# Kernel optimization log

Measured on AMD Instinct MI355X. Metric: run time of the kernel, lower is better.

The kernel has to match this reference:

```python
import jax, jax.numpy as jnp
import numpy as np

NUM_HEADS = 16
ROPE_THETA = 10000.0


def _rope_angles(seq_len, head_dim, dtype):
    # lucidrains rotary_embedding_torch: freqs = theta^(-2i/d) for i in 0..d/2,
    # angles = pos * freq, then each angle repeated twice along last dim (interleaved pairs).
    inv_freq = 1.0 / (ROPE_THETA ** (jnp.arange(0, head_dim, 2, dtype=jnp.float32) / head_dim))
    angles = jnp.arange(seq_len, dtype=jnp.float32)[:, None] * inv_freq  # [N, D/2]
    return jnp.repeat(angles, 2, axis=-1).astype(dtype)  # [N, D]


def _rotate_half(t):
    # interleaved pairs: (x0, x1) -> (-x1, x0)
    t1 = t[..., ::2]
    t2 = t[..., 1::2]
    return jnp.stack([-t2, t1], axis=-1).reshape(t.shape)


def _apply_rope(t, cos, sin):
    # t: [B, H, N, D]; cos/sin: [N, D]
    return t * cos + _rotate_half(t) * sin


def setup_inputs() -> dict:
    key = jax.random.key(0)
    ks = jax.random.split(key, 5)
    B, N, C = 4, 1024, 1024
    return {
        "x": jax.random.normal(ks[0], (B, N, C), dtype=jnp.float32),
        "w_qkv": jax.random.normal(ks[1], (C, 3 * C), dtype=jnp.float32) * (C ** -0.5),
        "b_qkv": jax.random.normal(ks[2], (3 * C,), dtype=jnp.float32) * 0.02,
        "w_proj": jax.random.normal(ks[3], (C, C), dtype=jnp.float32) * (C ** -0.5),
        "b_proj": jax.random.normal(ks[4], (C,), dtype=jnp.float32) * 0.02,
    }


def reference(x, w_qkv, b_qkv, w_proj, b_proj):
    B, N, C = x.shape
    H = NUM_HEADS
    D = C // H

    qkv = x @ w_qkv + b_qkv  # [B, N, 3C]
    qkv = qkv.reshape(B, N, 3, H, D).transpose(2, 0, 3, 1, 4)  # [3, B, H, N, D]
    q, k, v = qkv[0], qkv[1], qkv[2]

    ang = _rope_angles(N, D, x.dtype)
    cos, sin = jnp.cos(ang), jnp.sin(ang)
    q = _apply_rope(q, cos, sin)
    k = _apply_rope(k, cos, sin)

    scale = D ** -0.5  # SDPA default scale
    scores = jnp.einsum("bhqd,bhkd->bhqk", q, k) * scale
    attn = jax.nn.softmax(scores, axis=-1)
    out = jnp.einsum("bhqk,bhkd->bhqd", attn, v)  # [B, H, N, D]

    out = out.transpose(0, 2, 1, 3).reshape(B, N, C)
    return out @ w_proj + b_proj
```

## Files before the change

### kernel.cpp

```cpp
#include <hip/hip_runtime.h>
#include <math.h>

#define BB 4
#define NN 1024
#define CC 1024
#define HH 16
#define DD 64
#define N3 3072

typedef __attribute__((ext_vector_type(8))) short bf16x8;
typedef __attribute__((ext_vector_type(8))) _Float16 f16x8;
typedef __attribute__((ext_vector_type(4))) _Float16 f16x4;
typedef __attribute__((ext_vector_type(4))) float f32x4;
typedef __attribute__((ext_vector_type(4))) unsigned int u32x4;
typedef __attribute__((ext_vector_type(2))) unsigned int u32x2;

struct ushort4_t { unsigned short x, y, z, w; };

static __device__ __forceinline__ unsigned short f2b(float f) {
    union { float f; unsigned int u; } v; v.f = f;
    unsigned int r = (v.u + 0x7fffu + ((v.u >> 16) & 1u)) >> 16;
    return (unsigned short)r;
}

static __device__ __forceinline__ void ldg_lds16(const void* g, void* l) {
    __builtin_amdgcn_global_load_lds(
        (const __attribute__((address_space(1))) unsigned int*)g,
        (__attribute__((address_space(3))) unsigned int*)l, 16, 0, 0);
}

static __device__ __forceinline__ void barx()  { asm volatile("s_barrier" ::: "memory"); }
static __device__ __forceinline__ void wlg0()  { asm volatile("s_waitcnt lgkmcnt(0)" ::: "memory");
                                                 __builtin_amdgcn_sched_barrier(0); }
static __device__ __forceinline__ void wvm8()  { asm volatile("s_waitcnt vmcnt(8)" ::: "memory"); }
static __device__ __forceinline__ void wvm4()  { asm volatile("s_waitcnt vmcnt(4)" ::: "memory"); }
static __device__ __forceinline__ void wvm0()  { asm volatile("s_waitcnt vmcnt(0)" ::: "memory"); }
static __device__ __forceinline__ void wnone() {}

__global__ __launch_bounds__(256) void prep(const float* __restrict__ x,
                                            const float* __restrict__ wq,
                                            const float* __restrict__ wp,
                                            _Float16* __restrict__ Xh,
                                            _Float16* __restrict__ Wqt,
                                            _Float16* __restrict__ Wpt,
                                            float* __restrict__ ct,
                                            float* __restrict__ st) {
    __shared__ __align__(16) _Float16 T[64][72];
    const int blk = blockIdx.x;
    const int t = threadIdx.x;
    if (blk < 4096) {
        int tid = blk * 256 + t;
        float4 v = ((const float4*)x)[tid];
        f16x4 o = {(_Float16)v.x, (_Float16)v.y, (_Float16)v.z, (_Float16)v.w};
        ((f16x4*)Xh)[tid] = o;
    } else if (blk < 5120) {
        const float* src; _Float16* dst; int ns, k0, n0;
        if (blk < 4864) {
            int idx = blk - 4096;
            k0 = (idx & 15) * 64; n0 = (idx >> 4) * 64;
            src = wq; dst = Wqt; ns = N3;
        } else {
            int idx = blk - 4864;
            k0 = (idx & 15) * 64; n0 = (idx >> 4) * 64;
            src = wp; dst = Wpt; ns = 1024;
        }
        {
            const int r  = t >> 2;
            const int cf = (t & 3) * 16;
            const float* sp = src + (size_t)(k0 + r) * ns + n0 + cf;
            float4 v0 = *(const float4*)(sp);
            float4 v1 = *(const float4*)(sp + 4);
            float4 v2 = *(const float4*)(sp + 8);
            float4 v3 = *(const float4*)(sp + 12);
            f16x8 a, b;
            a[0]=(_Float16)v0.x; a[1]=(_Float16)v0.y; a[2]=(_Float16)v0.z; a[3]=(_Float16)v0.w;
            a[4]=(_Float16)v1.x; a[5]=(_Float16)v1.y; a[6]=(_Float16)v1.z; a[7]=(_Float16)v1.w;
            b[0]=(_Float16)v2.x; b[1]=(_Float16)v2.y; b[2]=(_Float16)v2.z; b[3]=(_Float16)v2.w;
            b[4]=(_Float16)v3.x; b[5]=(_Float16)v3.y; b[6]=(_Float16)v3.z; b[7]=(_Float16)v3.w;
            *(f16x8*)&T[r][cf]     = a;
            *(f16x8*)&T[r][cf + 8] = b;
        }
        __syncthreads();
        {
            const int n  = t >> 2;
            const int kc = t & 3;
            f16x8 o0, o1;
            #pragma unroll
            for (int kk = 0; kk < 8; kk++) o0[kk] = T[kc * 16 + kk][n];
            #pragma unroll
            for (int kk = 0; kk < 8; kk++) o1[kk] = T[kc * 16 + 8 + kk][n];
            _Float16* dp = dst + (size_t)(n0 + n) * 1024 + k0 + kc * 16;
            *(f16x8*)dp       = o0;
            *(f16x8*)(dp + 8) = o1;
        }
    } else {
        int tid = (blk - 5120) * 256 + t;
        int n = tid >> 5, i = tid & 31;
        double ang = (double)n * exp2(-(double)i * (13.287712379549449 / 32.0));
        ct[tid] = (float)cos(ang);
        st[tid] = (float)sin(ang);
    }
}

__global__ __launch_bounds__(512, 2) void qkv_mfma(const _Float16* __restrict__ Ah,
                                                   const _Float16* __restrict__ Bt,
                                                   const float* __restrict__ bias,
                                                   const float* __restrict__ cost,
                                                   const float* __restrict__ sint,
                                                   unsigned short* __restrict__ Q,
                                                   unsigned short* __restrict__ K,
                                                   unsigned short* __restrict__ Vtg) {
    __shared__ __align__(16) _Float16 LA[4][128 * 64];
    __shared__ __align__(16) _Float16 LB[4][128 * 64];

    const int t    = threadIdx.x;
    const int lane = t & 63;
    const int w    = t >> 6;
    const int ln   = lane & 15, qd = lane >> 4;
    const int n0   = blockIdx.x * 256;
    const int m0   = blockIdx.y * 256;
    const int wm   = (w >> 2) * 128;
    const int wn   = (w & 3) * 64;

    const int L0 = t >> 3, hc0 = (t & 7) ^ (L0 & 7);
    const int row0 = 2 * L0 + (hc0 >> 2), co0 = (hc0 & 3) * 16;
    const int pp = 512 + t;
    const int L1 = pp >> 3, hc1 = (pp & 7) ^ (L1 & 7);
    const int row1 = 2 * L1 + (hc1 >> 2), co1 = (hc1 & 3) * 16;

    const char* gA = (const char*)Ah;
    const char* gB = (const char*)Bt;
    const size_t aof0 = (size_t)(m0 + row0) * 2048 + co0;
    const size_t aof1 = (size_t)(m0 + row1) * 2048 + co1;
    const size_t bof0 = (size_t)(n0 + row0) * 2048 + co0;
    const size_t bof1 = (size_t)(n0 + row1) * 2048 + co1;
    const int ld0 = (w * 64) * 8;
    const int ld1 = (512 + w * 64) * 8;

#define STAGE_A(kk, SLOT) { ldg_lds16(gA + aof0 + (size_t)(kk) * 64, &LA[SLOT][ld0]); \
                            ldg_lds16(gA + aof1 + (size_t)(kk) * 64, &LA[SLOT][ld1]); }
#define STAGE_B(kk, SLOT) { ldg_lds16(gB + bof0 + (size_t)(kk) * 64, &LB[SLOT][ld0]); \
                            ldg_lds16(gB + bof1 + (size_t)(kk) * 64, &LB[SLOT][ld1]); }

    STAGE_A(0, 0); STAGE_B(0, 0);
    STAGE_A(1, 1); STAGE_B(1, 1);
    STAGE_A(2, 2); STAGE_B(2, 2);
    wvm8();
    barx();

    f32x4 acc[8][4];
    #pragma unroll
    for (int i = 0; i < 8; i++)
        #pragma unroll
        for (int j = 0; j < 4; j++) acc[i][j] = (f32x4){0.f, 0.f, 0.f, 0.f};

    auto frag = [&](const _Float16* Lb, int r, int c) -> f16x8 {
        int idx = ((r >> 1) << 6) + ((((((r & 1) << 2) | c)) ^ ((r >> 1) & 7)) << 3);
        return *(const f16x8*)&Lb[idx];
    };

#define QK_TILE(kk, SLOT, STG, WAITFN) {                                            \
    const _Float16* Ab = LA[SLOT];                                                  \
    const _Float16* Bb = LB[SLOT];                                                  \
    f16x8 af[4], bf[4];                                                             \
    _Pragma("unroll") for (int i = 0; i < 4; i++) af[i] = frag(Ab, wm + i * 16 + ln, qd); \
    _Pragma("unroll") for (int j = 0; j < 4; j++) bf[j] = frag(Bb, wn + j * 16 + ln, qd); \
    if (STG) STAGE_A((kk) + 3, ((kk) + 3) & 3);                                     \
    barx(); wlg0();                                                                 \
    __builtin_amdgcn_s_setprio(1);                                                  \
    _Pragma("unroll") for (int i = 0; i < 4; i++)                                   \
        _Pragma("unroll") for (int j = 0; j < 4; j++)                               \
            acc[i][j] = __builtin_amdgcn_mfma_f32_16x16x32_f16(af[i], bf[j], acc[i][j], 0, 0, 0); \
    __builtin_amdgcn_s_setprio(0);                                                  \
    barx();                                                                         \
    _Pragma("unroll") for (int i = 0; i < 4; i++) af[i] = frag(Ab, wm + 64 + i * 16 + ln, qd); \
    if (STG) STAGE_B((kk) + 3, ((kk) + 3) & 3);                                     \
    WAITFN();                                                                       \
    barx(); wlg0();                                                                 \
    __builtin_amdgcn_s_setprio(1);                                                  \
    _Pragma("unroll") for (int i = 0; i < 4; i++)                                   \
        _Pragma("unroll") for (int j = 0; j < 4; j++)                               \
            acc[4 + i][j] = __builtin_amdgcn_mfma_f32_16x16x32_f16(af[i], bf[j], acc[4 + i][j], 0, 0, 0); \
    __builtin_amdgcn_s_setprio(0);                                                  \
    barx();                                                                         \
}

    for (int k = 0; k < 28; k += 4) {
        QK_TILE(k + 0, 0, 1, wvm8);
        QK_TILE(k + 1, 1, 1, wvm8);
        QK_TILE(k + 2, 2, 1, wvm8);
        QK_TILE(k + 3, 3, 1, wvm8);
    }
    QK_TILE(28, 0, 1, wvm8);
    QK_TILE(29, 1, 0, wvm4);
    QK_TILE(30, 2, 0, wvm0);
    QK_TILE(31, 3, 0, wnone);

#undef QK_TILE
#undef STAGE_A
#undef STAGE_B

    float* LW = (float*)(&LA[0][0]) + w * (16 * 68);
    const int s = (n0 + wn) >> 10;
    const int h = ((n0 + wn) >> 6) & 15;
    const int erow = lane >> 2;
    const int ec0  = (lane & 3) * 16;

    if (s < 2) {
        unsigned short* dst = (s == 0) ? Q : K;
        const float sc0 = (s == 0) ? 0.125f : 1.0f;
        f32x4 bb0 = *(const f32x4*)&bias[n0 + wn + ec0 + 0];
        f32x4 bb1 = *(const f32x4*)&bias[n0 + wn + ec0 + 4];
        f32x4 bb2 = *(const f32x4*)&bias[n0 + wn + ec0 + 8];
        f32x4 bb3 = *(const f32x4*)&bias[n0 + wn + ec0 + 12];
        #pragma unroll
        for (int i = 0; i < 8; i++) {
            #pragma unroll
            for (int j = 0; j < 4; j++)
                #pragma unroll
                for (int reg = 0; reg < 4; reg++)
                    LW[(qd * 4 + reg) * 68 + j * 16 + ln] = acc[i][j][reg];
            wlg0();
            f32x4 v0 = *(const f32x4*)&LW[erow * 68 + ec0 + 0];
            f32x4 v1 = *(const f32x4*)&LW[erow * 68 + ec0 + 4];
            f32x4 v2 = *(const f32x4*)&LW[erow * 68 + ec0 + 8];
            f32x4 v3 = *(const f32x4*)&LW[erow * 68 + ec0 + 12];
            wlg0();
            int row = m0 + wm + i * 16 + erow;
            int b = row >> 10, n = row & 1023;
            f32x4 cs0 = *(const f32x4*)&cost[n * 32 + (ec0 >> 1)];
            f32x4 cs1 = *(const f32x4*)&cost[n * 32 + (ec0 >> 1) + 4];
            f32x4 sn0 = *(const f32x4*)&sint[n * 32 + (ec0 >> 1)];
            f32x4 sn1 = *(const f32x4*)&sint[n * 32 + (ec0 >> 1) + 4];
            cs0 *= sc0; cs1 *= sc0; sn0 *= sc0; sn1 *= sc0;
            v0 += bb0; v1 += bb1; v2 += bb2; v3 += bb3;
            unsigned int pk0, pk1, pk2, pk3, pk4, pk5, pk6, pk7;
#define RP(PK, ve, vo, cs, sn) { float oe = (ve) * (cs) - (vo) * (sn);              \
                                 float oo = (vo) * (cs) + (ve) * (sn);              \
            asm("v_cvt_pk_bf16_f32 %0, %1, %2" : "=v"(PK) : "v"(oe), "v"(oo)); }
            RP(pk0, v0[0], v0[1], cs0[0], sn0[0]);
            RP(pk1, v0[2], v0[3], cs0[1], sn0[1]);
            RP(pk2, v1[0], v1[1], cs0[2], sn0[2]);
            RP(pk3, v1[2], v1[3], cs0[3], sn0[3]);
            RP(pk4, v2[0], v2[1], cs1[0], sn1[0]);
            RP(pk5, v2[2], v2[3], cs1[1], sn1[1]);
            RP(pk6, v3[0], v3[1], cs1[2], sn1[2]);
            RP(pk7, v3[2], v3[3], cs1[3], sn1[3]);
#undef RP
            unsigned short* op = dst + (((size_t)(b * HH + h)) * NN + n) * DD + ec0;
            u32x4 o0; o0[0] = pk0; o0[1] = pk1; o0[2] = pk2; o0[3] = pk3;
            u32x4 o1; o1[0] = pk4; o1[1] = pk5; o1[2] = pk6; o1[3] = pk7;
            *(u32x4*)op = o0;
            *(u32x4*)(op + 8) = o1;
        }
    } else {
        const float bb = bias[n0 + wn + lane];
        #pragma unroll
        for (int i = 0; i < 8; i++) {
            #pragma unroll
            for (int j = 0; j < 4; j++)
                #pragma unroll
                for (int reg = 0; reg < 4; reg++)
                    LW[(qd * 4 + reg) * 68 + j * 16 + ln] = acc[i][j][reg];
            wlg0();
            float e0  = LW[ 0 * 68 + lane] + bb, e1  = LW[ 1 * 68 + lane] + bb;
            float e2  = LW[ 2 * 68 + lane] + bb, e3  = LW[ 3 * 68 + lane] + bb;
            float e4  = LW[ 4 * 68 + lane] + bb, e5  = LW[ 5 * 68 + lane] + bb;
            float e6  = LW[ 6 * 68 + lane] + bb, e7  = LW[ 7 * 68 + lane] + bb;
            float e8  = LW[ 8 * 68 + lane] + bb, e9  = LW[ 9 * 68 + lane] + bb;
            float e10 = LW[10 * 68 + lane] + bb, e11 = LW[11 * 68 + lane] + bb;
            float e12 = LW[12 * 68 + lane] + bb, e13 = LW[13 * 68 + lane] + bb;
            float e14 = LW[14 * 68 + lane] + bb, e15 = LW[15 * 68 + lane] + bb;
            wlg0();
            unsigned int pk0, pk1, pk2, pk3, pk4, pk5, pk6, pk7;
#define CV(PK, a, b_) asm("v_cvt_pk_bf16_f32 %0, %1, %2" : "=v"(PK) : "v"(a), "v"(b_))
            CV(pk0, e0,  e1);  CV(pk1, e2,  e3);
            CV(pk2, e4,  e5);  CV(pk3, e6,  e7);
            CV(pk4, e8,  e9);  CV(pk5, e10, e11);
            CV(pk6, e12, e13); CV(pk7, e14, e15);
#undef CV
            int row0v = m0 + wm + i * 16;
            int b = row0v >> 10, nn = row0v & 1023;
            unsigned short* vp = Vtg + ((size_t)(b * HH + h) * DD + lane) * NN + nn;
            u32x4 o0; o0[0] = pk0; o0[1] = pk1; o0[2] = pk2; o0[3] = pk3;
            u32x4 o1; o1[0] = pk4; o1[1] = pk5; o1[2] = pk6; o1[3] = pk7;
            *(u32x4*)vp = o0;
            *(u32x4*)(vp + 8) = o1;
        }
    }
}

static __device__ __forceinline__ void gemm_body_pipe_n64(const char* gA, const char* gB,
                                                          int m0, int n0,
                                                          _Float16* As0, _Float16* As1,
                                                          _Float16* Bs0, _Float16* Bs1,
                                                          int tid, int ln, int qd,
                                                          int wm, int wn, f32x4 acc[4][2]) {
    const int lrow   = tid >> 3;
    const int lchunk = tid & 7;
    const int swz    = (lchunk ^ (lrow & 7)) * 8;

    u32x4 pa[4], pb[2];

    #pragma unroll
    for (int c = 0; c < 4; c++)
        pa[c] = *(const u32x4*)(gA + (size_t)(m0 + c * 32 + lrow) * 2048 + lchunk * 16);
    #pragma unroll
    for (int c = 0; c < 2; c++)
        pb[c] = *(const u32x4*)(gB + (size_t)(n0 + c * 32 + lrow) * 2048 + lchunk * 16);
    #pragma unroll
    for (int c = 0; c < 4; c++)
        *(u32x4*)&As0[(c * 32 + lrow) * 64 + swz] = pa[c];
    #pragma unroll
    for (int c = 0; c < 2; c++)
        *(u32x4*)&Bs0[(c * 32 + lrow) * 64 + swz] = pb[c];
    #pragma unroll
    for (int c = 0; c < 4; c++)
        pa[c] = *(const u32x4*)(gA + (size_t)(m0 + c * 32 + lrow) * 2048 + 128 + lchunk * 16);
    #pragma unroll
    for (int c = 0; c < 2; c++)
        pb[c] = *(const u32x4*)(gB + (size_t)(n0 + c * 32 + lrow) * 2048 + 128 + lchunk * 16);
    __syncthreads();

    #pragma unroll
    for (int t = 0; t < 16; t++) {
        const _Float16* Ac = (t & 1) ? As1 : As0;
        const _Float16* Bc = (t & 1) ? Bs1 : Bs0;

        #pragma unroll
        for (int kc = 0; kc < 2; kc++) {
            f16x8 af[4], bf[2];
            #pragma unroll
            for (int i = 0; i < 4; i++)
                af[i] = *(const f16x8*)&Ac[(wm + i * 16 + ln) * 64 +
                                           (((kc * 4 + qd) ^ (ln & 7)) * 8)];
            #pragma unroll
            for (int j = 0; j < 2; j++)
                bf[j] = *(const f16x8*)&Bc[(wn + j * 16 + ln) * 64 +
                                           (((kc * 4 + qd) ^ (ln & 7)) * 8)];
            #pragma unroll
            for (int i = 0; i < 4; i++)
                #pragma unroll
                for (int j = 0; j < 2; j++)
                    acc[i][j] = __builtin_amdgcn_mfma_f32_16x16x32_f16(af[i], bf[j],
                                                                       acc[i][j], 0, 0, 0);
        }

        if (t < 15) {
            _Float16* An = (t & 1) ? As0 : As1;
            _Float16* Bn = (t & 1) ? Bs0 : Bs1;
            #pragma unroll
            for (int c = 0; c < 4; c++)
                *(u32x4*)&An[(c * 32 + lrow) * 64 + swz] = pa[c];
            #pragma unroll
            for (int c = 0; c < 2; c++)
                *(u32x4*)&Bn[(c * 32 + lrow) * 64 + swz] = pb[c];
            if (t < 14) {
                size_t ko = (size_t)(t + 2) * 128;
                #pragma unroll
                for (int c = 0; c < 4; c++)
                    pa[c] = *(const u32x4*)(gA + (size_t)(m0 + c * 32 + lrow) * 2048 + ko + lchunk * 16);
                #pragma unroll
                for (int c = 0; c < 2; c++)
                    pb[c] = *(const u32x4*)(gB + (size_t)(n0 + c * 32 + lrow) * 2048 + ko + lchunk * 16);
            }
        }
        __syncthreads();
    }
}

__global__ __launch_bounds__(256, 2) void attn_flash(const unsigned short* __restrict__ Qb,
                                                     const unsigned short* __restrict__ Kb,
                                                     const unsigned short* __restrict__ Vtg,
                                                     _Float16* __restrict__ AO) {
    __shared__ __align__(16) unsigned short Ps[4][32 * 64];

    const int t    = threadIdx.x;
    const int lane = t & 63;
    const int w    = t >> 6;
    const int ln   = lane & 15;
    const int qd   = lane >> 4;

    const int lin  = blockIdx.x;
    const int slot = lin >> 3;
    const int hb   = (lin & 7) + 8 * (slot & 7);
    const int bq   = slot >> 3;
    const int h    = hb & 15;
    const int b    = hb >> 4;

    const size_t base = (size_t)(b * HH + h) * NN * DD;
    const char* Kc = (const char*)(Kb + base);
    const char* Vc = (const char*)(Vtg + base);

    bf16x8 qf[2][2];
    #pragma unroll
    for (int g = 0; g < 2; g++) {
        const unsigned short* qp = Qb + base +
            (size_t)(bq * 128 + w * 32 + g * 16 + ln) * DD + qd * 8;
        qf[g][0] = *(const bf16x8*)qp;
        qf[g][1] = *(const bf16x8*)(qp + 32);
    }

    f32x4 o[2][5];
    #pragma unroll
    for (int g = 0; g < 2; g++)
        #pragma unroll
        for (int x = 0; x < 5; x++) o[g][x] = (f32x4){0.f, 0.f, 0.f, 0.f};

    bf16x8 onesf;
    #pragma unroll
    for (int x = 0; x < 8; x++) onesf[x] = (short)0x3F80;

    const char* kbase = Kc + (size_t)ln * 128 + qd * 16;
    const char* vbase = Vc + (size_t)ln * 2048 + qd * 16;

    const float C1 = 1.44269504f;
    const float C0 = -16.0f * 1.44269504f;
    const int swp = 2 * (ln & 7);
    unsigned short* PsB = &Ps[w][0];

    bf16x8 ka[8], kb2[8], va[8];
    #pragma unroll
    for (int j = 0; j < 4; j++) {
        ka[2 * j]     = *(const bf16x8*)(kbase + j * 2048);
        ka[2 * j + 1] = *(const bf16x8*)(kbase + j * 2048 + 64);
    }

    auto iter = [&](int tt, bf16x8 (&kc)[8], bf16x8 (&kn)[8]) {
        if (tt < 15) {
            const char* kp = kbase + (size_t)(tt + 1) * 8192;
            #pragma unroll
            for (int j = 0; j < 4; j++) {
                kn[2 * j]     = *(const bf16x8*)(kp + j * 2048);
                kn[2 * j + 1] = *(const bf16x8*)(kp + j * 2048 + 64);
            }
        }
        {
            const char* vp = vbase + (size_t)tt * 128;
            #pragma unroll
            for (int j = 0; j < 4; j++) {
                va[2 * j]     = *(const bf16x8*)(vp + (size_t)j * 32768);
                va[2 * j + 1] = *(const bf16x8*)(vp + (size_t)j * 32768 + 64);
            }
        }
        f32x4 s[2][4];
        __builtin_amdgcn_s_setprio(1);
        #pragma unroll
        for (int j = 0; j < 4; j++)
            #pragma unroll
            for (int g = 0; g < 2; g++) {
                f32x4 sj = {0.f, 0.f, 0.f, 0.f};
                sj = __builtin_amdgcn_mfma_f32_16x16x32_bf16(kc[2 * j],     qf[g][0], sj, 0, 0, 0);
                sj = __builtin_amdgcn_mfma_f32_16x16x32_bf16(kc[2 * j + 1], qf[g][1], sj, 0, 0, 0);
                s[g][j] = sj;
            }
        __builtin_amdgcn_s_setprio(0);
        #pragma unroll
        for (int g = 0; g < 2; g++) {
            char* rowp = (char*)PsB + (g * 16 + ln) * 128;
            #pragma unroll
            for (int j = 0; j < 4; j++) {
                float p0, p1, p2, p3;
                float x0 = fmaf(s[g][j][0], C1, C0);
                float x1 = fmaf(s[g][j][1], C1, C0);
                float x2 = fmaf(s[g][j][2], C1, C0);
                float x3 = fmaf(s[g][j][3], C1, C0);
                asm("v_exp_f32 %0, %1" : "=v"(p0) : "v"(x0));
                asm("v_exp_f32 %0, %1" : "=v"(p1) : "v"(x1));
                asm("v_exp_f32 %0, %1" : "=v"(p2) : "v"(x2));
                asm("v_exp_f32 %0, %1" : "=v"(p3) : "v"(x3));
                unsigned int lo, hi;
                asm("v_cvt_pk_bf16_f32 %0, %1, %2" : "=v"(lo) : "v"(p0), "v"(p1));
                asm("v_cvt_pk_bf16_f32 %0, %1, %2" : "=v"(hi) : "v"(p2), "v"(p3));
                u32x2 pk; pk[0] = lo; pk[1] = hi;
                *(u32x2*)(rowp + (((4 * j + qd) ^ swp) * 8)) = pk;
            }
        }
        bf16x8 pf[2][2];
        #pragma unroll
        for (int g = 0; g < 2; g++) {
            pf[g][0] = *(const bf16x8*)&PsB[(g * 16 + ln) * 64 + ((qd ^ (ln & 7)) * 8)];
            pf[g][1] = *(const bf16x8*)&PsB[(g * 16 + ln) * 64 + (((4 + qd) ^ (ln & 7)) * 8)];
        }
        __builtin_amdgcn_s_setprio(1);
        #pragma unroll
        for (int j = 0; j < 4; j++)
            #pragma unroll
            for (int g = 0; g < 2; g++) {
                o[g][j] = __builtin_amdgcn_mfma_f32_16x16x32_bf16(pf[g][0], va[2 * j],     o[g][j], 0, 0, 0);
                o[g][j] = __builtin_amdgcn_mfma_f32_16x16x32_bf16(pf[g][1], va[2 * j + 1], o[g][j], 0, 0, 0);
            }
        #pragma unroll
        for (int g = 0; g < 2; g++) {
            o[g][4] = __builtin_amdgcn_mfma_f32_16x16x32_bf16(pf[g][0], onesf, o[g][4], 0, 0, 0);
            o[g][4] = __builtin_amdgcn_mfma_f32_16x16x32_bf16(pf[g][1], onesf, o[g][4], 0, 0, 0);
        }
        __builtin_amdgcn_s_setprio(0);
    };

    #pragma unroll
    for (int tp = 0; tp < 8; tp++) {
        iter(2 * tp,     ka,  kb2);
        iter(2 * tp + 1, kb2, ka);
    }

    #pragma unroll
    for (int g = 0; g < 2; g++)
        #pragma unroll
        for (int r = 0; r < 4; r++) {
            float inv = __builtin_amdgcn_rcpf(o[g][4][r]);
            int q = bq * 128 + w * 32 + g * 16 + qd * 4 + r;
            _Float16* op = AO + (((size_t)b * NN + q) * HH + h) * DD + ln;
            op[0]  = (_Float16)(o[g][0][r] * inv);
            op[16] = (_Float16)(o[g][1][r] * inv);
            op[32] = (_Float16)(o[g][2][r] * inv);
            op[48] = (_Float16)(o[g][3][r] * inv);
        }
}

__global__ __launch_bounds__(256) void proj_mfma(const _Float16* __restrict__ Ah,
                                                 const _Float16* __restrict__ Bt,
                                                 const float* __restrict__ bias,
                                                 float* __restrict__ out) {
    __shared__ __align__(16) _Float16 As[2][128 * 64];
    __shared__ __align__(16) _Float16 Bs[2][64 * 64];
    const int t = threadIdx.x;
    const int lane = t & 63;
    const int w = t >> 6;
    const int ln = lane & 15, qd = lane >> 4;
    const int n0 = blockIdx.x * 64;
    const int m0 = blockIdx.y * 128;
    const int wm = (w >> 1) * 64, wn = (w & 1) * 32;

    f32x4 acc[4][2];
    #pragma unroll
    for (int i = 0; i < 4; i++)
        #pragma unroll
        for (int j = 0; j < 2; j++) acc[i][j] = (f32x4){0.f, 0.f, 0.f, 0.f};

    gemm_body_pipe_n64((const char*)Ah, (const char*)Bt, m0, n0,
                       As[0], As[1], Bs[0], Bs[1], t, ln, qd, wm, wn, acc);

    #pragma unroll
    for (int i = 0; i < 4; i++) {
        #pragma unroll
        for (int reg = 0; reg < 4; reg++) {
            int row = m0 + wm + i * 16 + qd * 4 + reg;
            #pragma unroll
            for (int j = 0; j < 2; j++) {
                int col = n0 + wn + j * 16 + ln;
                out[(size_t)row * 1024 + col] = acc[i][j][reg] + bias[col];
            }
        }
    }
}

extern "C" void kernel_launch(void* const* d_in, const int* in_sizes, int n_in,
                              void* d_out, int out_size, void* d_ws, size_t ws_size,
                              hipStream_t stream) {
    const float* x      = (const float*)d_in[0];
    const float* w_qkv  = (const float*)d_in[1];
    const float* b_qkv  = (const float*)d_in[2];
    const float* w_proj = (const float*)d_in[3];
    const float* b_proj = (const float*)d_in[4];
    float* out = (float*)d_out;

    char* ws = (char*)d_ws;
    _Float16* Xh   = (_Float16*)(ws);
    _Float16* Wqt  = (_Float16*)(ws + (8u << 20));
    _Float16* Wpt  = (_Float16*)(ws + (14u << 20));
    unsigned short* Q  = (unsigned short*)(ws + (16u << 20));
    unsigned short* K  = (unsigned short*)(ws + (24u << 20));
    unsigned short* Vt = (unsigned short*)(ws + (32u << 20));
    _Float16* AOh  = (_Float16*)(ws + (40u << 20));
    float* cost    = (float*)(ws + (48u << 20));
    float* sint    = (float*)(ws + (48u << 20) + (128u << 10));

    prep<<<5248, 256, 0, stream>>>(x, w_qkv, w_proj, Xh, Wqt, Wpt, cost, sint);
    qkv_mfma<<<dim3(12, 16), 512, 0, stream>>>(Xh, Wqt, b_qkv, cost, sint, Q, K, Vt);
    attn_flash<<<512, 256, 0, stream>>>(Q, K, Vt, AOh);
    proj_mfma<<<dim3(16, 32), 256, 0, stream>>>(AOh, Wpt, b_proj, out);
}
```

Before: 196.9 us.

## Stage K and V tiles through double-buffered LDS with direct global-to-LDS loads

The attention kernel previously had every wave load its own copy of each K and V tile from global memory into registers. It now stages each 64x64 K and V tile once per block into swizzled, double-buffered shared memory using direct global-to-LDS loads, with a wait and barrier per tile, and each wave reads its fragments from LDS. This cuts duplicate global and L2 traffic and register pressure, which allows launch bounds to rise from 2 to 3 blocks per CU. In exchange it adds two block barriers per tile and LDS read traffic, and occupancy is limited by the larger LDS footprint.

```diff
diff --git a/kernel.cpp b/kernel.cpp
--- a/kernel.cpp
+++ b/kernel.cpp
@@ -369,10 +369,12 @@
     }
 }
 
-__global__ __launch_bounds__(256, 2) void attn_flash(const unsigned short* __restrict__ Qb,
+__global__ __launch_bounds__(256, 3) void attn_flash(const unsigned short* __restrict__ Qb,
                                                      const unsigned short* __restrict__ Kb,
                                                      const unsigned short* __restrict__ Vtg,
                                                      _Float16* __restrict__ AO) {
+    __shared__ __align__(16) unsigned short Ks[2][64 * 64];
+    __shared__ __align__(16) unsigned short Vt[2][64 * 64];
     __shared__ __align__(16) unsigned short Ps[4][32 * 64];
 
     const int t    = threadIdx.x;
@@ -391,6 +393,9 @@
     const size_t base = (size_t)(b * HH + h) * NN * DD;
     const char* Kc = (const char*)(Kb + base);
     const char* Vc = (const char*)(Vtg + base);
+    const int xorc = ((lane & 7) ^ (lane >> 3)) * 16;
+    const int r8   = lane >> 3;
+    const int wrow = w * 16;
 
     bf16x8 qf[2][2];
     #pragma unroll
@@ -411,50 +416,49 @@
     #pragma unroll
     for (int x = 0; x < 8; x++) onesf[x] = (short)0x3F80;
 
-    const char* kbase = Kc + (size_t)ln * 128 + qd * 16;
-    const char* vbase = Vc + (size_t)ln * 2048 + qd * 16;
+#define STAGE_K(tile, buf) {                                                     \
+    _Pragma("unroll") for (int c = 0; c < 2; c++) {                              \
+        int rr = wrow + c * 8 + r8;                                              \
+        ldg_lds16(Kc + (size_t)((tile) * 64 + rr) * 128 + xorc,                  \
+                  &Ks[buf][(wrow + c * 8) * 64]);                                \
+    } }
+#define STAGE_V(tile, buf) {                                                     \
+    _Pragma("unroll") for (int c = 0; c < 2; c++) {                              \
+        int rr = wrow + c * 8 + r8;                                              \
+        ldg_lds16(Vc + (size_t)rr * 2048 + (size_t)(tile) * 128 + xorc,          \
+                  &Vt[buf][(wrow + c * 8) * 64]);                                \
+    } }
+
+    STAGE_K(0, 0); STAGE_V(0, 0);
+    STAGE_K(1, 1); STAGE_V(1, 1);
 
     const float C1 = 1.44269504f;
     const float C0 = -16.0f * 1.44269504f;
     const int swp = 2 * (ln & 7);
     unsigned short* PsB = &Ps[w][0];
 
-    bf16x8 ka[8], kb2[8], va[8];
-    #pragma unroll
-    for (int j = 0; j < 4; j++) {
-        ka[2 * j]     = *(const bf16x8*)(kbase + j * 2048);
-        ka[2 * j + 1] = *(const bf16x8*)(kbase + j * 2048 + 64);
-    }
-
-    auto iter = [&](int tt, bf16x8 (&kc)[8], bf16x8 (&kn)[8]) {
-        if (tt < 15) {
-            const char* kp = kbase + (size_t)(tt + 1) * 8192;
-            #pragma unroll
-            for (int j = 0; j < 4; j++) {
-                kn[2 * j]     = *(const bf16x8*)(kp + j * 2048);
-                kn[2 * j + 1] = *(const bf16x8*)(kp + j * 2048 + 64);
-            }
-        }
-        {
-            const char* vp = vbase + (size_t)tt * 128;
-            #pragma unroll
-            for (int j = 0; j < 4; j++) {
-                va[2 * j]     = *(const bf16x8*)(vp + (size_t)j * 32768);
-                va[2 * j + 1] = *(const bf16x8*)(vp + (size_t)j * 32768 + 64);
-            }
-        }
+    #pragma unroll
+    for (int tt = 0; tt < 16; tt++) {
+        if (tt < 15) wvm4(); else wvm0();
+        barx();
+
+        const unsigned short* KsB = Ks[tt & 1];
+        const unsigned short* VtB = Vt[tt & 1];
+
         f32x4 s[2][4];
-        __builtin_amdgcn_s_setprio(1);
-        #pragma unroll
-        for (int j = 0; j < 4; j++)
+        #pragma unroll
+        for (int j = 0; j < 4; j++) {
+            bf16x8 k0f = *(const bf16x8*)&KsB[(ln + 16 * j) * 64 + ((qd ^ (ln & 7)) * 8)];
+            bf16x8 k1f = *(const bf16x8*)&KsB[(ln + 16 * j) * 64 + (((4 + qd) ^ (ln & 7)) * 8)];
             #pragma unroll
             for (int g = 0; g < 2; g++) {
                 f32x4 sj = {0.f, 0.f, 0.f, 0.f};
-                sj = __builtin_amdgcn_mfma_f32_16x16x32_bf16(kc[2 * j],     qf[g][0], sj, 0, 0, 0);
-                sj = __builtin_amdgcn_mfma_f32_16x16x32_bf16(kc[2 * j + 1], qf[g][1], sj, 0, 0, 0);
+                sj = __builtin_amdgcn_mfma_f32_16x16x32_bf16(k0f, qf[g][0], sj, 0, 0, 0);
+                sj = __builtin_amdgcn_mfma_f32_16x16x32_bf16(k1f, qf[g][1], sj, 0, 0, 0);
                 s[g][j] = sj;
             }
-        __builtin_amdgcn_s_setprio(0);
+        }
+
         #pragma unroll
         for (int g = 0; g < 2; g++) {
             char* rowp = (char*)PsB + (g * 16 + ln) * 128;
@@ -476,33 +480,43 @@
                 *(u32x2*)(rowp + (((4 * j + qd) ^ swp) * 8)) = pk;
             }
         }
-        bf16x8 pf[2][2];
-        #pragma unroll
-        for (int g = 0; g < 2; g++) {
-            pf[g][0] = *(const bf16x8*)&PsB[(g * 16 + ln) * 64 + ((qd ^ (ln & 7)) * 8)];
-            pf[g][1] = *(const bf16x8*)&PsB[(g * 16 + ln) * 64 + (((4 + qd) ^ (ln & 7)) * 8)];
-        }
-        __builtin_amdgcn_s_setprio(1);
-        #pragma unroll
-        for (int j = 0; j < 4; j++)
+
+        {
+            bf16x8 pf[2][2];
             #pragma unroll
             for (int g = 0; g < 2; g++) {
-                o[g][j] = __builtin_amdgcn_mfma_f32_16x16x32_bf16(pf[g][0], va[2 * j],     o[g][j], 0, 0, 0);
-                o[g][j] = __builtin_amdgcn_mfma_f32_16x16x32_bf16(pf[g][1], va[2 * j + 1], o[g][j], 0, 0, 0);
-            }
-        #pragma unroll
-        for (int g = 0; g < 2; g++) {
-            o[g][4] = __builtin_amdgcn_mfma_f32_16x16x32_bf16(pf[g][0], onesf, o[g][4], 0, 0, 0);
-            o[g][4] = __builtin_amdgcn_mfma_f32_16x16x32_bf16(pf[g][1], onesf, o[g][4], 0, 0, 0);
-        }
-        __builtin_amdgcn_s_setprio(0);
-    };
-
-    #pragma unroll
-    for (int tp = 0; tp < 8; tp++) {
-        iter(2 * tp,     ka,  kb2);
-        iter(2 * tp + 1, kb2, ka);
-    }
+                pf[g][0] = *(const bf16x8*)&PsB[(g * 16 + ln) * 64 + ((qd ^ (ln & 7)) * 8)];
+                pf[g][1] = *(const bf16x8*)&PsB[(g * 16 + ln) * 64 + (((4 + qd) ^ (ln & 7)) * 8)];
+            }
+            __builtin_amdgcn_s_setprio(1);
+            #pragma unroll
+            for (int j = 0; j < 4; j++) {
+                bf16x8 v0f = *(const bf16x8*)&VtB[(ln + 16 * j) * 64 + ((qd ^ (ln & 7)) * 8)];
+                bf16x8 v1f = *(const bf16x8*)&VtB[(ln + 16 * j) * 64 + (((4 + qd) ^ (ln & 7)) * 8)];
+                #pragma unroll
+                for (int g = 0; g < 2; g++) {
+                    o[g][j] = __builtin_amdgcn_mfma_f32_16x16x32_bf16(pf[g][0], v0f, o[g][j], 0, 0, 0);
+                    o[g][j] = __builtin_amdgcn_mfma_f32_16x16x32_bf16(pf[g][1], v1f, o[g][j], 0, 0, 0);
+                }
+            }
+            #pragma unroll
+            for (int g = 0; g < 2; g++) {
+                o[g][4] = __builtin_amdgcn_mfma_f32_16x16x32_bf16(pf[g][0], onesf, o[g][4], 0, 0, 0);
+                o[g][4] = __builtin_amdgcn_mfma_f32_16x16x32_bf16(pf[g][1], onesf, o[g][4], 0, 0, 0);
+            }
+            __builtin_amdgcn_s_setprio(0);
+        }
+
+        barx();
+
+        if (tt < 14) {
+            STAGE_K(tt + 2, tt & 1);
+            STAGE_V(tt + 2, tt & 1);
+        }
+    }
+
+#undef STAGE_K
+#undef STAGE_V
 
     #pragma unroll
     for (int g = 0; g < 2; g++)
```

Result: faster. 164.7 us (-16.4%).
